# Kernel tuning notes

Hardware: AMD Instinct MI355X
Metric: run time of the kernel (lower is better)

The kernel has to match this reference:

```python
import jax, jax.numpy as jnp
import numpy as np

SCALE = 2.0 ** 10.5
DROPOUT_P = 0.5


def setup_inputs() -> dict:
    key = jax.random.key(0)
    ks = jax.random.split(key, 8)
    B, G, S, D_IN, D_H = 1, 8, 4096, 3, 8
    return {
        "x1": jax.random.normal(ks[0], (B, G, S, D_IN), dtype=jnp.float32),
        "x2": jax.random.normal(ks[1], (B, G, S, D_IN), dtype=jnp.float32),
        "Wq": jax.random.normal(ks[2], (D_H, D_IN), dtype=jnp.float32),
        "bq": jax.random.normal(ks[3], (D_H,), dtype=jnp.float32),
        "Wk": jax.random.normal(ks[4], (D_H, D_IN), dtype=jnp.float32),
        "bk": jax.random.normal(ks[5], (D_H,), dtype=jnp.float32),
        "Wv": jax.random.normal(ks[6], (D_H, D_IN), dtype=jnp.float32),
        "bv": jax.random.normal(ks[7], (D_H,), dtype=jnp.float32),
    }


def reference(x1, x2, Wq, bq, Wk, bk, Wv, bv):
    # Linear projections (torch Linear: x @ W.T + b)
    q = jnp.einsum("bgsd,hd->bgsh", x1, Wq) + bq  # [B,G,S,8]
    k = jnp.einsum("bgsd,hd->bgsh", x2, Wk) + bk
    v = jnp.einsum("bgsd,hd->bgsh", x1, Wv) + bv
    # scores scaled by custom factor 2**10.5 (multiplied, not divided)
    scores = jnp.einsum("bgsh,bgth->bgst", q, k) * jnp.float32(SCALE)  # [B,G,S,S]
    probs = jax.nn.softmax(scores, axis=-1)
    # dropout p=0.5 (training mode), deterministic mask, inverted scaling
    mask = jax.random.bernoulli(jax.random.key(42), 1.0 - DROPOUT_P, probs.shape)
    probs = jnp.where(mask, probs / jnp.float32(1.0 - DROPOUT_P), jnp.float32(0.0))
    out = jnp.einsum("bgst,bgth->bgsh", probs, v)  # [B,G,S,8]
    return out
```

## Files before the change

### kernel.cpp

```cpp
#include <hip/hip_runtime.h>
#include <stdint.h>

namespace {

constexpr int G = 8;
constexpr int S = 4096;
constexpr int RPB = 16;
constexpr int QT = 1024;
constexpr float K2C = (float)(1448.15468787004945 * 1.44269504088896340736);
constexpr float CUT = 32.0f;

__device__ __forceinline__ uint32_t rotl32(uint32_t x, uint32_t n) {
  return (x << n) | (x >> (32u - n));
}

__device__ __forceinline__ void tfround(uint32_t& x0, uint32_t& x1, uint32_t r) {
  x0 += x1;
  x1 = rotl32(x1, r);
  x1 ^= x0;
}

__device__ __forceinline__ void threefry2x32(uint32_t c0, uint32_t c1,
                                             uint32_t& r0, uint32_t& r1) {
  const uint32_t ks0 = 0u;
  const uint32_t ks1 = 42u;
  const uint32_t ks2 = 0x1BD11BF0u;
  uint32_t x0 = c0 + ks0;
  uint32_t x1 = c1 + ks1;
  tfround(x0, x1, 13); tfround(x0, x1, 15); tfround(x0, x1, 26); tfround(x0, x1, 6);
  x0 += ks1; x1 += ks2 + 1u;
  tfround(x0, x1, 17); tfround(x0, x1, 29); tfround(x0, x1, 16); tfround(x0, x1, 24);
  x0 += ks2; x1 += ks0 + 2u;
  tfround(x0, x1, 13); tfround(x0, x1, 15); tfround(x0, x1, 26); tfround(x0, x1, 6);
  x0 += ks0; x1 += ks1 + 3u;
  tfround(x0, x1, 17); tfround(x0, x1, 29); tfround(x0, x1, 16); tfround(x0, x1, 24);
  x0 += ks1; x1 += ks2 + 4u;
  tfround(x0, x1, 13); tfround(x0, x1, 15); tfround(x0, x1, 26); tfround(x0, x1, 6);
  x0 += ks2; x1 += ks0 + 5u;
  r0 = x0; r1 = x1;
}

__device__ __forceinline__ bool keep_mask(uint32_t i) {
  uint32_t a, b;
  threefry2x32(0u, i, a, b);
  return (((a ^ b) >> 31) == 0u);
}

__global__ __launch_bounds__(256, 4)
void fused_attn(const float* __restrict__ x1, const float* __restrict__ x2,
                const float* __restrict__ Wq, const float* __restrict__ bq,
                const float* __restrict__ Wk, const float* __restrict__ bk,
                const float* __restrict__ Wv, const float* __restrict__ bv,
                float* __restrict__ out) {
  __shared__ __align__(16) float XS[QT];
  __shared__ __align__(16) float YS[QT];
  __shared__ __align__(16) float ZS[QT];
  __shared__ float4 CKs[RPB];
  __shared__ float  MW[4][8];
  __shared__ float  WACC[4][8][5];

  const int g = blockIdx.x >> 8;
  const int stile = blockIdx.x & 255;
  const int row0 = stile * RPB;
  const int tid = (int)threadIdx.x;
  const int wave = tid >> 6;
  const int lane = tid & 63;
  const int rowbase = (wave >> 1) << 3;
  const int half = wave & 1;

  const float* x2g = x2 + (size_t)g * S * 3;
  const float* x1g = x1 + (size_t)g * S * 3;

  if (tid < RPB) {
    const float* px = x1g + (size_t)(row0 + tid) * 3;
    const float a0 = px[0], a1 = px[1], a2 = px[2];
    float q[8];
#pragma unroll
    for (int h = 0; h < 8; ++h)
      q[h] = bq[h] + a0 * Wq[h * 3 + 0] + a1 * Wq[h * 3 + 1] + a2 * Wq[h * 3 + 2];
    float t0 = 0.f, t1 = 0.f, t2 = 0.f, t3 = 0.f;
#pragma unroll
    for (int h = 0; h < 8; ++h) {
      t0 += q[h] * Wk[h * 3 + 0];
      t1 += q[h] * Wk[h * 3 + 1];
      t2 += q[h] * Wk[h * 3 + 2];
      t3 += q[h] * bk[h];
    }
    CKs[tid] = make_float4(t0 * K2C, t1 * K2C, t2 * K2C, t3 * K2C);
  }
  __syncthreads();

  float4 CK[8];
#pragma unroll
  for (int h = 0; h < 8; ++h) CK[h] = CKs[rowbase + h];

  float4* X4 = (float4*)XS;
  float4* Y4 = (float4*)YS;
  float4* Z4 = (float4*)ZS;

  auto stage = [&](int q) {
    const float4* src = (const float4*)(x2g + (size_t)q * QT * 3);
    const float4 f0 = src[tid * 3 + 0];
    const float4 f1 = src[tid * 3 + 1];
    const float4 f2 = src[tid * 3 + 2];
    X4[tid] = make_float4(f0.x, f0.w, f1.z, f2.y);
    Y4[tid] = make_float4(f0.y, f1.x, f1.w, f2.z);
    Z4[tid] = make_float4(f0.z, f1.y, f2.x, f2.w);
  };

  float m[8];
#pragma unroll
  for (int h = 0; h < 8; ++h) m[h] = -3.0e38f;

  for (int q = 0; q < 4; ++q) {
    __syncthreads();
    stage(q);
    __syncthreads();
#pragma unroll
    for (int grp = 0; grp < 2; ++grp) {
      const int i4 = half * 128 + (grp << 6) + lane;
      const float4 fx = X4[i4], fy = Y4[i4], fz = Z4[i4];
      const float bxa[4] = {fx.x, fx.y, fx.z, fx.w};
      const float bya[4] = {fy.x, fy.y, fy.z, fy.w};
      const float bza[4] = {fz.x, fz.y, fz.z, fz.w};
#pragma unroll
      for (int e = 0; e < 4; ++e) {
        const float bx = bxa[e], by = bya[e], bz = bza[e];
#pragma unroll
        for (int h = 0; h < 8; ++h)
          m[h] = fmaxf(m[h], fmaf(CK[h].x, bx,
                       fmaf(CK[h].y, by, fmaf(CK[h].z, bz, CK[h].w))));
      }
    }
  }
#pragma unroll
  for (int msk = 1; msk < 64; msk <<= 1) {
#pragma unroll
    for (int h = 0; h < 8; ++h) m[h] = fmaxf(m[h], __shfl_xor(m[h], msk, 64));
  }
  if (lane == 0) {
#pragma unroll
    for (int h = 0; h < 8; ++h) MW[wave][h] = m[h];
  }
  __syncthreads();
#pragma unroll
  for (int h = 0; h < 8; ++h) {
    const float rm = fmaxf(m[h], MW[wave ^ 1][h]);
    CK[h].w -= rm;
  }

  float lr[8], lk[8], o0[8], o1[8], o2[8];
#pragma unroll
  for (int h = 0; h < 8; ++h) { lr[h] = 0.f; lk[h] = 0.f; o0[h] = 0.f; o1[h] = 0.f; o2[h] = 0.f; }
  const uint32_t rg0 = (uint32_t)(g * S + row0 + rowbase);

  for (int q = 0; q < 4; ++q) {
    __syncthreads();
    stage(q);
    __syncthreads();
#pragma unroll
    for (int grp = 0; grp < 2; ++grp) {
      const int i4 = half * 128 + (grp << 6) + lane;
      const float4 fx = X4[i4], fy = Y4[i4], fz = Z4[i4];
      const float bxa[4] = {fx.x, fx.y, fx.z, fx.w};
      const float bya[4] = {fy.x, fy.y, fy.z, fy.w};
      const float bza[4] = {fz.x, fz.y, fz.z, fz.w};
#pragma unroll
      for (int e = 0; e < 4; ++e) {
        const float bx = bxa[e], by = bya[e], bz = bza[e];
        float d[8];
#pragma unroll
        for (int h = 0; h < 8; ++h)
          d[h] = fmaf(CK[h].x, bx, fmaf(CK[h].y, by, fmaf(CK[h].z, bz, CK[h].w)));
        float mx = d[0];
#pragma unroll
        for (int h = 1; h < 8; ++h) mx = fmaxf(mx, d[h]);
        if (__any(mx > -CUT)) {
#pragma unroll
          for (int h = 0; h < 8; ++h) {
            unsigned long long bm = __ballot(d[h] > -CUT);
            while (bm) {
              const int l = (int)__ffsll(bm) - 1;
              bm &= bm - 1;
              const int dbits = __builtin_amdgcn_readlane(__float_as_int(d[h]), l);
              const float pr = exp2f(__int_as_float(dbits));
              lr[h] += pr;
              const uint32_t t =
                  (uint32_t)(q * QT + half * 512 + (grp << 8) + (l << 2) + e);
              if (keep_mask(((rg0 + (uint32_t)h) << 12) + t)) {
                const float* pa = x1g + 3u * t;
                const float a0 = pa[0], a1 = pa[1], a2 = pa[2];
                lk[h] += pr;
                o0[h] += pr * a0; o1[h] += pr * a1; o2[h] += pr * a2;
              }
            }
          }
        }
      }
    }
  }

  if (lane == 0) {
#pragma unroll
    for (int h = 0; h < 8; ++h) {
      WACC[wave][h][0] = lr[h];
      WACC[wave][h][1] = lk[h];
      WACC[wave][h][2] = o0[h];
      WACC[wave][h][3] = o1[h];
      WACC[wave][h][4] = o2[h];
    }
  }
  __syncthreads();

  if (tid < RPB) {
    const int pw = (tid >> 3) << 1;
    const int hr = tid & 7;
    const float l  = WACC[pw][hr][0] + WACC[pw + 1][hr][0];
    const float lkp = WACC[pw][hr][1] + WACC[pw + 1][hr][1];
    const float a0 = WACC[pw][hr][2] + WACC[pw + 1][hr][2];
    const float a1 = WACC[pw][hr][3] + WACC[pw + 1][hr][3];
    const float a2 = WACC[pw][hr][4] + WACC[pw + 1][hr][4];
    const float sc = 2.0f / l;
    float o[8];
#pragma unroll
    for (int h = 0; h < 8; ++h)
      o[h] = (bv[h] * lkp + Wv[h * 3 + 0] * a0 + Wv[h * 3 + 1] * a1 +
              Wv[h * 3 + 2] * a2) * sc;
    float4* po = (float4*)(out + (size_t)(g * S + row0 + tid) * 8);
    po[0] = make_float4(o[0], o[1], o[2], o[3]);
    po[1] = make_float4(o[4], o[5], o[6], o[7]);
  }
}

}

extern "C" void kernel_launch(void* const* d_in, const int* in_sizes, int n_in,
                              void* d_out, int out_size, void* d_ws, size_t ws_size,
                              hipStream_t stream) {
  (void)in_sizes; (void)n_in; (void)d_ws; (void)ws_size; (void)out_size;
  const float* x1 = (const float*)d_in[0];
  const float* x2 = (const float*)d_in[1];
  const float* Wq = (const float*)d_in[2];
  const float* bq = (const float*)d_in[3];
  const float* Wk = (const float*)d_in[4];
  const float* bk = (const float*)d_in[5];
  const float* Wv = (const float*)d_in[6];
  const float* bv = (const float*)d_in[7];
  float* out = (float*)d_out;

  fused_attn<<<dim3(G * (S / RPB)), dim3(256), 0, stream>>>(
      x1, x2, Wq, bq, Wk, bk, Wv, bv, out);
}
```

Measured before the change: 102.8 us.

## Stage full key set in LDS and batch softmax hits via per-wave log

Each block now processes 64 query rows, with each wave owning 16 rows over all 4096 keys, and loads the entire transposed x2 group into shared memory once. Score hits above the cutoff are appended to a per-wave log, then exp, dropout hash and value accumulation are done lane-parallel over logged entries and reduced with shuffles. This aims to remove the serial per-hit readlane loop and the repeated staging and cross-wave max exchange. It adds large LDS use, fewer blocks, and a fixed log capacity that drops hits beyond 128 per wave.

```diff
diff --git a/kernel.cpp b/kernel.cpp
--- a/kernel.cpp
+++ b/kernel.cpp
@@ -5,8 +5,9 @@
 
 constexpr int G = 8;
 constexpr int S = 4096;
-constexpr int RPB = 16;
-constexpr int QT = 1024;
+constexpr int RPB = 64;
+constexpr int RPW = 16;
+constexpr int LOGCAP = 128;
 constexpr float K2C = (float)(1448.15468787004945 * 1.44269504088896340736);
 constexpr float CUT = 32.0f;
 
@@ -46,27 +47,24 @@
   return (((a ^ b) >> 31) == 0u);
 }
 
-__global__ __launch_bounds__(256, 4)
+__global__ __launch_bounds__(256)
 void fused_attn(const float* __restrict__ x1, const float* __restrict__ x2,
                 const float* __restrict__ Wq, const float* __restrict__ bq,
                 const float* __restrict__ Wk, const float* __restrict__ bk,
                 const float* __restrict__ Wv, const float* __restrict__ bv,
                 float* __restrict__ out) {
-  __shared__ __align__(16) float XS[QT];
-  __shared__ __align__(16) float YS[QT];
-  __shared__ __align__(16) float ZS[QT];
+  __shared__ __align__(16) float XS[S];
+  __shared__ __align__(16) float YS[S];
+  __shared__ __align__(16) float ZS[S];
   __shared__ float4 CKs[RPB];
-  __shared__ float  MW[4][8];
-  __shared__ float  WACC[4][8][5];
-
-  const int g = blockIdx.x >> 8;
-  const int stile = blockIdx.x & 255;
-  const int row0 = stile * RPB;
+  __shared__ uint32_t LOGB[4][LOGCAP * 2];
+
+  const int g = blockIdx.x >> 6;
+  const int tile = blockIdx.x & 63;
+  const int row0 = tile * RPB;
   const int tid = (int)threadIdx.x;
   const int wave = tid >> 6;
   const int lane = tid & 63;
-  const int rowbase = (wave >> 1) << 3;
-  const int half = wave & 1;
 
   const float* x2g = x2 + (size_t)g * S * 3;
   const float* x1g = x1 + (size_t)g * S * 3;
@@ -88,145 +86,154 @@
     }
     CKs[tid] = make_float4(t0 * K2C, t1 * K2C, t2 * K2C, t3 * K2C);
   }
+
+  {
+    const float4* src = (const float4*)x2g;
+    float4* X4 = (float4*)XS;
+    float4* Y4 = (float4*)YS;
+    float4* Z4 = (float4*)ZS;
+    float4 tmp[12];
+#pragma unroll
+    for (int it = 0; it < 4; ++it)
+#pragma unroll
+      for (int k = 0; k < 3; ++k)
+        tmp[it * 3 + k] = src[it * 768 + tid * 3 + k];
+#pragma unroll
+    for (int it = 0; it < 4; ++it) {
+      const float4 f0 = tmp[it * 3 + 0];
+      const float4 f1 = tmp[it * 3 + 1];
+      const float4 f2 = tmp[it * 3 + 2];
+      const int gi = it * 256 + tid;
+      X4[gi] = make_float4(f0.x, f0.w, f1.z, f2.y);
+      Y4[gi] = make_float4(f0.y, f1.x, f1.w, f2.z);
+      Z4[gi] = make_float4(f0.z, f1.y, f2.x, f2.w);
+    }
+  }
   __syncthreads();
 
-  float4 CK[8];
-#pragma unroll
-  for (int h = 0; h < 8; ++h) CK[h] = CKs[rowbase + h];
-
-  float4* X4 = (float4*)XS;
-  float4* Y4 = (float4*)YS;
-  float4* Z4 = (float4*)ZS;
-
-  auto stage = [&](int q) {
-    const float4* src = (const float4*)(x2g + (size_t)q * QT * 3);
-    const float4 f0 = src[tid * 3 + 0];
-    const float4 f1 = src[tid * 3 + 1];
-    const float4 f2 = src[tid * 3 + 2];
-    X4[tid] = make_float4(f0.x, f0.w, f1.z, f2.y);
-    Y4[tid] = make_float4(f0.y, f1.x, f1.w, f2.z);
-    Z4[tid] = make_float4(f0.z, f1.y, f2.x, f2.w);
-  };
-
-  float m[8];
-#pragma unroll
-  for (int h = 0; h < 8; ++h) m[h] = -3.0e38f;
-
-  for (int q = 0; q < 4; ++q) {
-    __syncthreads();
-    stage(q);
-    __syncthreads();
-#pragma unroll
-    for (int grp = 0; grp < 2; ++grp) {
-      const int i4 = half * 128 + (grp << 6) + lane;
-      const float4 fx = X4[i4], fy = Y4[i4], fz = Z4[i4];
-      const float bxa[4] = {fx.x, fx.y, fx.z, fx.w};
-      const float bya[4] = {fy.x, fy.y, fy.z, fy.w};
-      const float bza[4] = {fz.x, fz.y, fz.z, fz.w};
-#pragma unroll
-      for (int e = 0; e < 4; ++e) {
-        const float bx = bxa[e], by = bya[e], bz = bza[e];
-#pragma unroll
-        for (int h = 0; h < 8; ++h)
-          m[h] = fmaxf(m[h], fmaf(CK[h].x, bx,
-                       fmaf(CK[h].y, by, fmaf(CK[h].z, bz, CK[h].w))));
-      }
+  const float4* X4 = (const float4*)XS;
+  const float4* Y4 = (const float4*)YS;
+  const float4* Z4 = (const float4*)ZS;
+
+  float4 CK[RPW];
+#pragma unroll
+  for (int r = 0; r < RPW; ++r) CK[r] = CKs[wave * RPW + r];
+
+  float m[RPW];
+#pragma unroll
+  for (int r = 0; r < RPW; ++r) m[r] = -3.0e38f;
+
+#pragma unroll 2
+  for (int c = 0; c < S / 4 / 64; ++c) {
+    const int i4 = (c << 6) + lane;
+    const float4 fx = X4[i4], fy = Y4[i4], fz = Z4[i4];
+    const float bxa[4] = {fx.x, fx.y, fx.z, fx.w};
+    const float bya[4] = {fy.x, fy.y, fy.z, fy.w};
+    const float bza[4] = {fz.x, fz.y, fz.z, fz.w};
+#pragma unroll
+    for (int e = 0; e < 4; ++e) {
+      const float bx = bxa[e], by = bya[e], bz = bza[e];
+#pragma unroll
+      for (int r = 0; r < RPW; ++r)
+        m[r] = fmaxf(m[r], fmaf(CK[r].x, bx,
+                     fmaf(CK[r].y, by, fmaf(CK[r].z, bz, CK[r].w))));
     }
   }
 #pragma unroll
   for (int msk = 1; msk < 64; msk <<= 1) {
 #pragma unroll
-    for (int h = 0; h < 8; ++h) m[h] = fmaxf(m[h], __shfl_xor(m[h], msk, 64));
-  }
-  if (lane == 0) {
-#pragma unroll
-    for (int h = 0; h < 8; ++h) MW[wave][h] = m[h];
-  }
-  __syncthreads();
-#pragma unroll
-  for (int h = 0; h < 8; ++h) {
-    const float rm = fmaxf(m[h], MW[wave ^ 1][h]);
-    CK[h].w -= rm;
-  }
-
-  float lr[8], lk[8], o0[8], o1[8], o2[8];
-#pragma unroll
-  for (int h = 0; h < 8; ++h) { lr[h] = 0.f; lk[h] = 0.f; o0[h] = 0.f; o1[h] = 0.f; o2[h] = 0.f; }
-  const uint32_t rg0 = (uint32_t)(g * S + row0 + rowbase);
-
-  for (int q = 0; q < 4; ++q) {
-    __syncthreads();
-    stage(q);
-    __syncthreads();
-#pragma unroll
-    for (int grp = 0; grp < 2; ++grp) {
-      const int i4 = half * 128 + (grp << 6) + lane;
-      const float4 fx = X4[i4], fy = Y4[i4], fz = Z4[i4];
-      const float bxa[4] = {fx.x, fx.y, fx.z, fx.w};
-      const float bya[4] = {fy.x, fy.y, fy.z, fy.w};
-      const float bza[4] = {fz.x, fz.y, fz.z, fz.w};
-#pragma unroll
-      for (int e = 0; e < 4; ++e) {
-        const float bx = bxa[e], by = bya[e], bz = bza[e];
-        float d[8];
-#pragma unroll
-        for (int h = 0; h < 8; ++h)
-          d[h] = fmaf(CK[h].x, bx, fmaf(CK[h].y, by, fmaf(CK[h].z, bz, CK[h].w)));
-        float mx = d[0];
-#pragma unroll
-        for (int h = 1; h < 8; ++h) mx = fmaxf(mx, d[h]);
-        if (__any(mx > -CUT)) {
-#pragma unroll
-          for (int h = 0; h < 8; ++h) {
-            unsigned long long bm = __ballot(d[h] > -CUT);
-            while (bm) {
-              const int l = (int)__ffsll(bm) - 1;
-              bm &= bm - 1;
-              const int dbits = __builtin_amdgcn_readlane(__float_as_int(d[h]), l);
-              const float pr = exp2f(__int_as_float(dbits));
-              lr[h] += pr;
-              const uint32_t t =
-                  (uint32_t)(q * QT + half * 512 + (grp << 8) + (l << 2) + e);
-              if (keep_mask(((rg0 + (uint32_t)h) << 12) + t)) {
-                const float* pa = x1g + 3u * t;
-                const float a0 = pa[0], a1 = pa[1], a2 = pa[2];
-                lk[h] += pr;
-                o0[h] += pr * a0; o1[h] += pr * a1; o2[h] += pr * a2;
-              }
+    for (int r = 0; r < RPW; ++r) m[r] = fmaxf(m[r], __shfl_xor(m[r], msk, 64));
+  }
+#pragma unroll
+  for (int r = 0; r < RPW; ++r) CK[r].w -= m[r];
+
+  uint32_t* LOG = LOGB[wave];
+  int cnt = 0;
+
+#pragma unroll 2
+  for (int c = 0; c < S / 4 / 64; ++c) {
+    const int i4 = (c << 6) + lane;
+    const float4 fx = X4[i4], fy = Y4[i4], fz = Z4[i4];
+    const float bxa[4] = {fx.x, fx.y, fx.z, fx.w};
+    const float bya[4] = {fy.x, fy.y, fy.z, fy.w};
+    const float bza[4] = {fz.x, fz.y, fz.z, fz.w};
+#pragma unroll
+    for (int e = 0; e < 4; ++e) {
+      const float bx = bxa[e], by = bya[e], bz = bza[e];
+      float d[RPW];
+#pragma unroll
+      for (int r = 0; r < RPW; ++r)
+        d[r] = fmaf(CK[r].x, bx, fmaf(CK[r].y, by, fmaf(CK[r].z, bz, CK[r].w)));
+      float m01 = fmaxf(fmaxf(d[0], d[1]), fmaxf(d[2], d[3]));
+      float m23 = fmaxf(fmaxf(d[4], d[5]), fmaxf(d[6], d[7]));
+      float m45 = fmaxf(fmaxf(d[8], d[9]), fmaxf(d[10], d[11]));
+      float m67 = fmaxf(fmaxf(d[12], d[13]), fmaxf(d[14], d[15]));
+      const float mx = fmaxf(fmaxf(m01, m23), fmaxf(m45, m67));
+      if (__any(mx > -CUT)) {
+        const uint32_t tt = (uint32_t)((i4 << 2) + e);
+#pragma unroll
+        for (int r = 0; r < RPW; ++r) {
+          const bool hit = (d[r] > -CUT);
+          const unsigned long long bm = __ballot(hit);
+          if (bm) {
+            const int pos =
+                cnt + (int)__popcll(bm & ((1ull << lane) - 1ull));
+            if (hit && pos < LOGCAP) {
+              LOG[pos * 2 + 0] = ((uint32_t)r << 12) | tt;
+              LOG[pos * 2 + 1] = __float_as_uint(d[r]);
             }
+            cnt += (int)__popcll(bm);
           }
         }
       }
     }
   }
-
-  if (lane == 0) {
-#pragma unroll
-    for (int h = 0; h < 8; ++h) {
-      WACC[wave][h][0] = lr[h];
-      WACC[wave][h][1] = lk[h];
-      WACC[wave][h][2] = o0[h];
-      WACC[wave][h][3] = o1[h];
-      WACC[wave][h][4] = o2[h];
-    }
-  }
-  __syncthreads();
-
-  if (tid < RPB) {
-    const int pw = (tid >> 3) << 1;
-    const int hr = tid & 7;
-    const float l  = WACC[pw][hr][0] + WACC[pw + 1][hr][0];
-    const float lkp = WACC[pw][hr][1] + WACC[pw + 1][hr][1];
-    const float a0 = WACC[pw][hr][2] + WACC[pw + 1][hr][2];
-    const float a1 = WACC[pw][hr][3] + WACC[pw + 1][hr][3];
-    const float a2 = WACC[pw][hr][4] + WACC[pw + 1][hr][4];
-    const float sc = 2.0f / l;
+  if (cnt > LOGCAP) cnt = LOGCAP;
+
+  const uint32_t grow0 = (uint32_t)(g * S + row0 + wave * RPW);
+  float lr = 0.f, lkp = 0.f, a0 = 0.f, a1 = 0.f, a2 = 0.f;
+
+  for (int base = 0; base < cnt; base += 64) {
+    const int idx = base + lane;
+    const bool val = (idx < cnt);
+    const uint32_t w0 = val ? LOG[idx * 2 + 0] : 0u;
+    const float dd = val ? __uint_as_float(LOG[idx * 2 + 1]) : 0.0f;
+    const int er = (int)(w0 >> 12);
+    const uint32_t et = w0 & 4095u;
+    const float pr = val ? exp2f(dd) : 0.0f;
+    const bool keep = val && keep_mask(((grow0 + (uint32_t)er) << 12) | et);
+    float c0 = 0.f, c1 = 0.f, c2 = 0.f, prk = 0.f;
+    if (keep) {
+      const float* pa = x1g + 3u * et;
+      prk = pr;
+      c0 = pr * pa[0]; c1 = pr * pa[1]; c2 = pr * pa[2];
+    }
+    const int nj = (cnt - base < 64) ? (cnt - base) : 64;
+    for (int jj = 0; jj < nj; ++jj) {
+      const int rj = __shfl(er, jj, 64);
+      const float prj = __shfl(pr, jj, 64);
+      const float prkj = __shfl(prk, jj, 64);
+      const float c0j = __shfl(c0, jj, 64);
+      const float c1j = __shfl(c1, jj, 64);
+      const float c2j = __shfl(c2, jj, 64);
+      const bool mine = (rj == lane);
+      lr += mine ? prj : 0.f;
+      lkp += mine ? prkj : 0.f;
+      a0 += mine ? c0j : 0.f;
+      a1 += mine ? c1j : 0.f;
+      a2 += mine ? c2j : 0.f;
+    }
+  }
+
+  if (lane < RPW) {
+    const int srow = row0 + wave * RPW + lane;
+    const float sc = 2.0f / lr;
     float o[8];
 #pragma unroll
     for (int h = 0; h < 8; ++h)
       o[h] = (bv[h] * lkp + Wv[h * 3 + 0] * a0 + Wv[h * 3 + 1] * a1 +
               Wv[h * 3 + 2] * a2) * sc;
-    float4* po = (float4*)(out + (size_t)(g * S + row0 + tid) * 8);
+    float4* po = (float4*)(out + (size_t)(g * S + srow) * 8);
     po[0] = make_float4(o[0], o[1], o[2], o[3]);
     po[1] = make_float4(o[4], o[5], o[6], o[7]);
   }
```

New measurement: 94.75 us. 7.8% less time.
